# Optimization experiments

Hardware: AMD Instinct MI355X
Metric: run time of the kernel (lower is better)

## Reference

```python
import jax, jax.numpy as jnp
import numpy as np

W_IMG, H_IMG = 800.0, 600.0          # BoxList.size (w, h)
BBOX_W = (10.0, 10.0, 5.0, 5.0)      # BoxCoder weights
BBOX_CLAMP = float(np.log(1000.0 / 16.0))
SCORE_THRESH = 0.05
NMS_THRESH = 0.5
TOPN_PER_CLS = 300
DET_PER_IMG = 100


def setup_inputs() -> dict:
    key = jax.random.key(0)
    kl, kb, kp, kf = jax.random.split(key, 4)
    B, N, C, D = 2, 512, 151, 4096
    # spread logits so softmax produces scores above the 0.05 threshold
    class_logits = jax.random.normal(kl, (B, N, C), jnp.float32) * 4.0
    box_regression = jax.random.normal(kb, (B, N, C * 4), jnp.float32) * 0.2
    # valid xyxy proposal boxes inside the image
    pts = jax.random.uniform(kp, (B, N, 2, 2), jnp.float32)
    pts = pts * jnp.array([W_IMG - 1.0, H_IMG - 1.0], jnp.float32)
    lo = jnp.min(pts, axis=2)
    hi = jnp.max(pts, axis=2)
    proposal_boxes = jnp.concatenate([lo, hi], axis=-1)
    features = jax.random.normal(kf, (B, N, D), jnp.float32)
    return {"class_logits": class_logits, "box_regression": box_regression,
            "proposal_boxes": proposal_boxes, "features": features}


def decode_boxes(reg, boxes):
    wx, wy, ww, wh = BBOX_W
    widths = boxes[..., 2] - boxes[..., 0] + 1.0
    heights = boxes[..., 3] - boxes[..., 1] + 1.0
    ctr_x = boxes[..., 0] + 0.5 * widths
    ctr_y = boxes[..., 1] + 0.5 * heights
    dx = reg[..., 0] / wx
    dy = reg[..., 1] / wy
    dw = jnp.minimum(reg[..., 2] / ww, BBOX_CLAMP)
    dh = jnp.minimum(reg[..., 3] / wh, BBOX_CLAMP)
    pcx = dx * widths[..., None] + ctr_x[..., None]
    pcy = dy * heights[..., None] + ctr_y[..., None]
    pw = jnp.exp(dw) * widths[..., None]
    ph = jnp.exp(dh) * heights[..., None]
    return jnp.stack([pcx - 0.5 * pw, pcy - 0.5 * ph,
                      pcx + 0.5 * pw - 1.0, pcy + 0.5 * ph - 1.0], axis=-1)


def pairwise_iou(b):
    area = (b[:, 2] - b[:, 0] + 1.0) * (b[:, 3] - b[:, 1] + 1.0)
    xx1 = jnp.maximum(b[:, None, 0], b[None, :, 0])
    yy1 = jnp.maximum(b[:, None, 1], b[None, :, 1])
    xx2 = jnp.minimum(b[:, None, 2], b[None, :, 2])
    yy2 = jnp.minimum(b[:, None, 3], b[None, :, 3])
    inter = jnp.maximum(xx2 - xx1 + 1.0, 0.0) * jnp.maximum(yy2 - yy1 + 1.0, 0.0)
    return inter / (area[:, None] + area[None, :] - inter)


def class_nms(boxes, scores, valid):
    # Greedy NMS over one class of one image; fixed-shape, returns keep mask in
    # the ORIGINAL proposal order. `valid` = score > SCORE_THRESH prefilter.
    N = scores.shape[0]
    order = jnp.argsort(-scores)
    b = jax.lax.stop_gradient(boxes[order])
    v = valid[order]
    iou = pairwise_iou(b)
    idx = jnp.arange(N)
    def body(i, keep):
        sup = (iou[i] > NMS_THRESH) & (idx > i) & keep[i]
        return keep & ~sup
    keep = jax.lax.fori_loop(0, N, body, v)
    keep = keep & (jnp.cumsum(keep) <= TOPN_PER_CLS)  # post-NMS per-class top-n
    return jnp.zeros(N, bool).at[order].set(keep)


def reference(class_logits, box_regression, proposal_boxes, features):
    B, N, C = class_logits.shape
    prob = jax.nn.softmax(class_logits, axis=-1)                 # [B,N,C]
    reg = box_regression.reshape(B, N, C, 4)
    boxes = decode_boxes(reg, proposal_boxes)                    # [B,N,C,4]
    # clip_to_image(remove_empty=False)
    x = jnp.clip(boxes[..., 0::2], 0.0, W_IMG - 1.0)
    y = jnp.clip(boxes[..., 1::2], 0.0, H_IMG - 1.0)
    boxes = jnp.stack([x[..., 0], y[..., 0], x[..., 1], y[..., 1]], axis=-1)
    valid = prob > SCORE_THRESH                                  # [B,N,C]
    # per-(image, class) NMS, vectorized via vmap
    boxes_c = jnp.swapaxes(boxes, 1, 2)                          # [B,C,N,4]
    scores_c = jnp.swapaxes(prob, 1, 2)                          # [B,C,N]
    valid_c = jnp.swapaxes(valid, 1, 2)
    keep_c = jax.vmap(jax.vmap(class_nms))(boxes_c, scores_c, valid_c)
    keep = jnp.swapaxes(keep_c, 1, 2)                            # [B,N,C]
    keep = keep & (jnp.arange(C)[None, None, :] != 0)            # drop background
    # nms_filter_duplicates: one (score, label) per proposal
    dist_scores = prob * keep
    labels = jnp.argmax(dist_scores, axis=-1)                    # [B,N]
    scores_pre = jnp.max(dist_scores, axis=-1)                   # [B,N]
    det_valid = scores_pre > 0
    # detections_per_img cap via kth-largest threshold (only if over the cap)
    num = jnp.sum(det_valid, axis=-1)                            # [B]
    kth = jax.lax.top_k(jnp.where(det_valid, scores_pre, -1.0), DET_PER_IMG)[0][:, -1]
    thr = jnp.where(num > DET_PER_IMG, kth, -1.0)
    det_valid = det_valid & (scores_pre >= thr[:, None])
    # gather box of the winning class: boxes_per_cls[final_inds, labels_pre]
    final_boxes = jnp.take_along_axis(boxes, labels[..., None, None], axis=2)[:, :, 0, :]
    final_boxes = jnp.where(det_valid[..., None], final_boxes, 0.0)
    final_scores = jnp.where(det_valid, scores_pre, 0.0)
    final_labels = jnp.where(det_valid, labels, 0)
    nms_features = features * det_valid[..., None]               # features[orig_inds]
    return final_boxes, final_scores, final_labels, det_valid, nms_features
```

## Files before the change

kernel.cpp:

```cpp
#include <hip/hip_runtime.h>
#include <math.h>

#define Bn 2
#define Nn 512
#define Cn 151
#define Dn 4096
#define W_IMG 800.0f
#define H_IMG 600.0f
#define SCORE_T 0.05f
#define NMS_T 0.5f
#define TOPN 300
#define DETMAX 100
#define BBOX_CLAMP 4.135166556742356f

#define OFF_BOXES  ((size_t)0)
#define OFF_SCORES ((size_t)(Bn * Nn * 4))
#define OFF_LABELS (OFF_SCORES + (size_t)(Bn * Nn))
#define OFF_VALID  (OFF_LABELS + (size_t)(Bn * Nn))
#define OFF_FEATS  (OFF_VALID + (size_t)(Bn * Nn))

__device__ __forceinline__ float4 decode_clip(const float4 pr, const float4 rg) {
  const float w = pr.z - pr.x + 1.0f;
  const float h = pr.w - pr.y + 1.0f;
  const float cx = pr.x + 0.5f * w;
  const float cy = pr.y + 0.5f * h;
  const float dx = rg.x / 10.0f;
  const float dy = rg.y / 10.0f;
  const float dw = fminf(rg.z / 5.0f, BBOX_CLAMP);
  const float dh = fminf(rg.w / 5.0f, BBOX_CLAMP);
  const float pcx = dx * w + cx;
  const float pcy = dy * h + cy;
  const float pw = expf(dw) * w;
  const float ph = expf(dh) * h;
  float x1 = pcx - 0.5f * pw;
  float y1 = pcy - 0.5f * ph;
  float x2 = pcx + 0.5f * pw - 1.0f;
  float y2 = pcy + 0.5f * ph - 1.0f;
  x1 = fminf(fmaxf(x1, 0.0f), W_IMG - 1.0f);
  x2 = fminf(fmaxf(x2, 0.0f), W_IMG - 1.0f);
  y1 = fminf(fmaxf(y1, 0.0f), H_IMG - 1.0f);
  y2 = fminf(fmaxf(y2, 0.0f), H_IMG - 1.0f);
  return make_float4(x1, y1, x2, y2);
}

__global__ void kA_softmax(const float* __restrict__ logits,
                           float* __restrict__ prob_t,
                           unsigned long long* __restrict__ packed) {
  const int wave = threadIdx.x >> 6;
  const int lane = threadIdx.x & 63;
  const int bn = blockIdx.x * 4 + wave;
  const int b = bn >> 9;
  const int n = bn & (Nn - 1);

  const float* lrow = logits + (size_t)bn * Cn;
  const float l0 = lrow[lane];
  const float l1 = lrow[lane + 64];
  const float l2 = (lane + 128 < Cn) ? lrow[lane + 128] : -INFINITY;

  float mx = fmaxf(l0, fmaxf(l1, l2));
  #pragma unroll
  for (int o = 32; o > 0; o >>= 1) mx = fmaxf(mx, __shfl_xor(mx, o));

  const float e0 = expf(l0 - mx);
  const float e1 = expf(l1 - mx);
  const float e2 = (lane + 128 < Cn) ? expf(l2 - mx) : 0.0f;
  float sum = e0 + e1 + e2;
  #pragma unroll
  for (int o = 32; o > 0; o >>= 1) sum += __shfl_xor(sum, o);
  const float inv = 1.0f / sum;

  float* pt = prob_t + (size_t)b * Cn * Nn + n;
  pt[(size_t)lane * Nn] = e0 * inv;
  pt[(size_t)(lane + 64) * Nn] = e1 * inv;
  if (lane + 128 < Cn) pt[(size_t)(lane + 128) * Nn] = e2 * inv;

  if (lane == 0) packed[bn] = 0ull;
}

__global__ void kB_nms(const float* __restrict__ prob_t,
                       const float* __restrict__ reg,
                       const float* __restrict__ props,
                       unsigned long long* __restrict__ packed) {
  const int bc = blockIdx.x;
  const int b = bc / Cn;
  const int c = bc % Cn;
  const int lane = threadIdx.x;
  if (c == 0) return;

  __shared__ float ls[Nn];
  __shared__ int   ln[Nn];
  __shared__ float ss2[64];
  __shared__ int   sn2[64];
  __shared__ float fs[Nn];
  __shared__ int   fn[Nn];
  __shared__ float fb[Nn][4];
  __shared__ unsigned char kp[Nn];

  const float* col = prob_t + ((size_t)b * Cn + c) * Nn;
  int base = 0;
  #pragma unroll
  for (int j = 0; j < Nn / 64; ++j) {
    const int n = j * 64 + lane;
    const float s = col[n];
    const bool v = s > SCORE_T;
    const unsigned long long m = __ballot(v);
    if (v) {
      const int pos = base + __popcll(m & ((1ull << lane) - 1ull));
      ls[pos] = s; ln[pos] = n;
    }
    base += __popcll(m);
  }
  const int M = base;
  if (M == 0) return;
  __syncthreads();

  if (M <= 64) {
    float s = -1.0f; int n = -1;
    if (lane < M) { s = ls[lane]; n = ln[lane]; }
    int rank = 0;
    for (int j = 0; j < M; ++j) {
      const float sj = __shfl(s, j);
      const int nj = __shfl(n, j);
      if (lane < M) rank += (sj > s) || (sj == s && nj < n);
    }
    if (lane < M) { ss2[rank] = s; sn2[rank] = n; }
    __syncthreads();

    float sc = 0.0f; int sn = 0;
    float x1 = 0.0f, y1 = 0.0f, x2 = 0.0f, y2 = 0.0f;
    if (lane < M) {
      sc = ss2[lane]; sn = sn2[lane];
      const int i = b * Nn + sn;
      const float4 pr = *(const float4*)(props + (size_t)i * 4);
      const float4 rg = *(const float4*)(reg + ((size_t)i * Cn + c) * 4);
      const float4 bx = decode_clip(pr, rg);
      x1 = bx.x; y1 = bx.y; x2 = bx.z; y2 = bx.w;
    }
    const float area = (x2 - x1 + 1.0f) * (y2 - y1 + 1.0f);

    unsigned long long live = (M >= 64) ? ~0ull : ((1ull << M) - 1ull);
    int i = 0;
    while (i < 64) {
      const unsigned long long rem = live & (~0ull << i);
      if (!rem) break;
      i = __ffsll(rem) - 1;
      const float ax1 = __shfl(x1, i), ay1 = __shfl(y1, i);
      const float ax2 = __shfl(x2, i), ay2 = __shfl(y2, i);
      const float aarea = (ax2 - ax1 + 1.0f) * (ay2 - ay1 + 1.0f);
      const float xx1 = fmaxf(ax1, x1), yy1 = fmaxf(ay1, y1);
      const float xx2 = fminf(ax2, x2), yy2 = fminf(ay2, y2);
      const float inter = fmaxf(xx2 - xx1 + 1.0f, 0.0f) * fmaxf(yy2 - yy1 + 1.0f, 0.0f);
      const float iou = inter / (aarea + area - inter);
      const bool sup = (lane > i) && (lane < M) && ((live >> lane) & 1ull) && (iou > NMS_T);
      live &= ~__ballot(sup);
      ++i;
    }
    if (lane < M && ((live >> lane) & 1ull)) {
      const unsigned long long key =
          ((unsigned long long)__float_as_uint(sc) << 32) | (unsigned int)(Cn - c);
      atomicMax(&packed[(size_t)b * Nn + sn], key);
    }
  } else {
    for (int i0 = lane; i0 < M; i0 += 64) {
      const float si = ls[i0]; const int ni = ln[i0];
      int r = 0;
      for (int j = 0; j < M; ++j) {
        const float sj = ls[j]; const int nj = ln[j];
        r += (sj > si) || (sj == si && nj < ni);
      }
      fs[r] = si; fn[r] = ni;
    }
    __syncthreads();
    for (int i0 = lane; i0 < M; i0 += 64) {
      const int i = b * Nn + fn[i0];
      const float4 pr = *(const float4*)(props + (size_t)i * 4);
      const float4 rg = *(const float4*)(reg + ((size_t)i * Cn + c) * 4);
      const float4 bx = decode_clip(pr, rg);
      fb[i0][0] = bx.x; fb[i0][1] = bx.y; fb[i0][2] = bx.z; fb[i0][3] = bx.w;
      kp[i0] = 1;
    }
    __syncthreads();
    for (int i = 0; i < M; ++i) {
      if (!kp[i]) continue;
      const float ax1 = fb[i][0], ay1 = fb[i][1], ax2 = fb[i][2], ay2 = fb[i][3];
      const float aarea = (ax2 - ax1 + 1.0f) * (ay2 - ay1 + 1.0f);
      for (int t = i + 1 + lane; t < M; t += 64) {
        if (kp[t]) {
          const float bx1 = fb[t][0], by1 = fb[t][1], bx2 = fb[t][2], by2 = fb[t][3];
          const float barea = (bx2 - bx1 + 1.0f) * (by2 - by1 + 1.0f);
          const float xx1 = fmaxf(ax1, bx1), yy1 = fmaxf(ay1, by1);
          const float xx2 = fminf(ax2, bx2), yy2 = fminf(ay2, by2);
          const float inter = fmaxf(xx2 - xx1 + 1.0f, 0.0f) * fmaxf(yy2 - yy1 + 1.0f, 0.0f);
          if (inter / (aarea + barea - inter) > NMS_T) kp[t] = 0;
        }
      }
      __syncthreads();
    }
    if (lane == 0) {
      int cnt = 0;
      for (int t = 0; t < M; ++t)
        if (kp[t]) { if (++cnt > TOPN) kp[t] = 0; }
    }
    __syncthreads();
    for (int t = lane; t < M; t += 64) {
      if (kp[t]) {
        const unsigned long long key =
            ((unsigned long long)__float_as_uint(fs[t]) << 32) | (unsigned int)(Cn - c);
        atomicMax(&packed[(size_t)b * Nn + fn[t]], key);
      }
    }
  }
}

__global__ void kC_final(const unsigned long long* __restrict__ packed,
                         const float* __restrict__ reg,
                         const float* __restrict__ props,
                         float* __restrict__ out) {
  const int b = blockIdx.x;
  const int n = threadIdx.x;
  __shared__ float v[Nn];
  __shared__ int wcnt[8];
  __shared__ float sThr;

  const unsigned long long p = packed[(size_t)b * Nn + n];
  const float s = __uint_as_float((unsigned int)(p >> 32));
  const int label = (p != 0ull) ? (Cn - (int)(p & 0xFFFFFFFFull)) : 0;
  const bool pos = (s > 0.0f);
  v[n] = pos ? s : -1.0f;

  const unsigned long long bal = __ballot(pos);
  if ((n & 63) == 0) wcnt[n >> 6] = __popcll(bal);
  __syncthreads();
  int num = 0;
  #pragma unroll
  for (int i = 0; i < 8; ++i) num += wcnt[i];

  if (num > DETMAX) {
    for (int k = 2; k <= Nn; k <<= 1) {
      for (int j = k >> 1; j > 0; j >>= 1) {
        const int ixj = n ^ j;
        if (ixj > n) {
          const bool up = ((n & k) == 0);
          const float a = v[n], bb = v[ixj];
          if (up != (a > bb) && a != bb) { v[n] = bb; v[ixj] = a; }
        }
        __syncthreads();
      }
    }
    if (n == 0) sThr = v[DETMAX - 1];
  } else {
    if (n == 0) sThr = -1.0f;
  }
  __syncthreads();

  const bool valid = pos && (s >= sThr);
  const int i = b * Nn + n;
  float4 ob = make_float4(0.0f, 0.0f, 0.0f, 0.0f);
  if (valid) {
    const float4 pr = *(const float4*)(props + (size_t)i * 4);
    const float4 rg = *(const float4*)(reg + ((size_t)i * Cn + label) * 4);
    ob = decode_clip(pr, rg);
  }
  *(float4*)(out + OFF_BOXES + (size_t)i * 4) = ob;
  out[OFF_SCORES + i] = valid ? s : 0.0f;
  out[OFF_LABELS + i] = valid ? (float)label : 0.0f;
  out[OFF_VALID + i] = valid ? 1.0f : 0.0f;
}

__global__ void kD_feats(const float* __restrict__ feats,
                         const float* __restrict__ valid,
                         float* __restrict__ out) {
  const int row = blockIdx.x;
  const float m = valid[row];
  const float4* fi = (const float4*)(feats + (size_t)row * Dn);
  float4* fo = (float4*)(out + (size_t)row * Dn);
  #pragma unroll 4
  for (int t = threadIdx.x; t < Dn / 4; t += 256) {
    float4 x = fi[t];
    x.x *= m; x.y *= m; x.z *= m; x.w *= m;
    fo[t] = x;
  }
}

extern "C" void kernel_launch(void* const* d_in, const int* in_sizes, int n_in,
                              void* d_out, int out_size, void* d_ws, size_t ws_size,
                              hipStream_t stream) {
  const float* logits = (const float*)d_in[0];
  const float* reg    = (const float*)d_in[1];
  const float* props  = (const float*)d_in[2];
  const float* feats  = (const float*)d_in[3];
  float* out = (float*)d_out;

  unsigned long long* packed = (unsigned long long*)d_ws;
  float* prob_t = (float*)(packed + Bn * Nn);

  kA_softmax<<<Bn * Nn / 4, 256, 0, stream>>>(logits, prob_t, packed);
  kB_nms<<<Bn * Cn, 64, 0, stream>>>(prob_t, reg, props, packed);
  kC_final<<<Bn, Nn, 0, stream>>>(packed, reg, props, out);
  kD_feats<<<Bn * Nn, 256, 0, stream>>>(feats, out + OFF_VALID, out + OFF_FEATS);
}
```

Measured before the change: 96.98 us.

## Fuse softmax, NMS, top-k threshold and feature masking into one persistent kernel

Replaces the four separate kernel launches with a single 256-block persistent kernel. The stages are separated by a hand-written grid barrier built on atomic arrive/release flags. The per-class compaction now uses ds_permute so candidates stay in registers, and the bitonic sort that found the detection cap is replaced by a byte-wise radix select over the score bits. This is meant to remove launch gaps and the intermediate kernel boundaries. The costs are spin-wait barriers, only one block per CU, and a reliance on all 256 blocks being co-resident; the feature copy also runs at lower occupancy.

Measured after the change: 113.2 us. 1.17x slower.

```diff
diff --git a/kernel.cpp b/kernel.cpp
--- a/kernel.cpp
+++ b/kernel.cpp
@@ -12,6 +12,7 @@
 #define TOPN 300
 #define DETMAX 100
 #define BBOX_CLAMP 4.135166556742356f
+#define NBLK 256
 
 #define OFF_BOXES  ((size_t)0)
 #define OFF_SCORES ((size_t)(Bn * Nn * 4))
@@ -43,242 +44,300 @@
   return make_float4(x1, y1, x2, y2);
 }
 
-__global__ void kA_softmax(const float* __restrict__ logits,
-                           float* __restrict__ prob_t,
-                           unsigned long long* __restrict__ packed) {
-  const int wave = threadIdx.x >> 6;
-  const int lane = threadIdx.x & 63;
-  const int bn = blockIdx.x * 4 + wave;
-  const int b = bn >> 9;
-  const int n = bn & (Nn - 1);
-
-  const float* lrow = logits + (size_t)bn * Cn;
-  const float l0 = lrow[lane];
-  const float l1 = lrow[lane + 64];
-  const float l2 = (lane + 128 < Cn) ? lrow[lane + 128] : -INFINITY;
-
-  float mx = fmaxf(l0, fmaxf(l1, l2));
-  #pragma unroll
-  for (int o = 32; o > 0; o >>= 1) mx = fmaxf(mx, __shfl_xor(mx, o));
-
-  const float e0 = expf(l0 - mx);
-  const float e1 = expf(l1 - mx);
-  const float e2 = (lane + 128 < Cn) ? expf(l2 - mx) : 0.0f;
-  float sum = e0 + e1 + e2;
-  #pragma unroll
-  for (int o = 32; o > 0; o >>= 1) sum += __shfl_xor(sum, o);
-  const float inv = 1.0f / sum;
-
-  float* pt = prob_t + (size_t)b * Cn * Nn + n;
-  pt[(size_t)lane * Nn] = e0 * inv;
-  pt[(size_t)(lane + 64) * Nn] = e1 * inv;
-  if (lane + 128 < Cn) pt[(size_t)(lane + 128) * Nn] = e2 * inv;
-
-  if (lane == 0) packed[bn] = 0ull;
+__device__ __forceinline__ void grid_barrier(unsigned* arrive, unsigned* release,
+                                             unsigned phase) {
+  __syncthreads();
+  if (threadIdx.x == 0) {
+    __threadfence();
+    atomicExch(&arrive[blockIdx.x], phase);
+  }
+  if (blockIdx.x == 0) {
+    const unsigned j = threadIdx.x;
+    while (atomicAdd(&arrive[j], 0u) != phase) __builtin_amdgcn_s_sleep(1);
+    __syncthreads();
+    if (threadIdx.x == 0) atomicExch(release, phase);
+  }
+  if (threadIdx.x == 0) {
+    while (atomicAdd(release, 0u) != phase) __builtin_amdgcn_s_sleep(1);
+    __threadfence();
+  }
+  __syncthreads();
 }
 
-__global__ void kB_nms(const float* __restrict__ prob_t,
-                       const float* __restrict__ reg,
-                       const float* __restrict__ props,
-                       unsigned long long* __restrict__ packed) {
-  const int bc = blockIdx.x;
-  const int b = bc / Cn;
-  const int c = bc % Cn;
-  const int lane = threadIdx.x;
-  if (c == 0) return;
-
-  __shared__ float ls[Nn];
-  __shared__ int   ln[Nn];
-  __shared__ float ss2[64];
-  __shared__ int   sn2[64];
-  __shared__ float fs[Nn];
-  __shared__ int   fn[Nn];
-  __shared__ float fb[Nn][4];
-  __shared__ unsigned char kp[Nn];
-
-  const float* col = prob_t + ((size_t)b * Cn + c) * Nn;
-  int base = 0;
-  #pragma unroll
-  for (int j = 0; j < Nn / 64; ++j) {
-    const int n = j * 64 + lane;
-    const float s = col[n];
-    const bool v = s > SCORE_T;
-    const unsigned long long m = __ballot(v);
-    if (v) {
-      const int pos = base + __popcll(m & ((1ull << lane) - 1ull));
-      ls[pos] = s; ln[pos] = n;
-    }
-    base += __popcll(m);
-  }
-  const int M = base;
-  if (M == 0) return;
-  __syncthreads();
-
-  if (M <= 64) {
-    float s = -1.0f; int n = -1;
-    if (lane < M) { s = ls[lane]; n = ln[lane]; }
-    int rank = 0;
-    for (int j = 0; j < M; ++j) {
-      const float sj = __shfl(s, j);
-      const int nj = __shfl(n, j);
-      if (lane < M) rank += (sj > s) || (sj == s && nj < n);
-    }
-    if (lane < M) { ss2[rank] = s; sn2[rank] = n; }
+struct FallbackWS {
+  float fs[Nn];
+  int   fn[Nn];
+  float fb[Nn][4];
+  unsigned char kp[Nn];
+};
+union SharedU {
+  FallbackWS fwb[2];
+  struct { unsigned hist[256]; int red[256]; unsigned dsel[2]; } p3;
+};
+
+__global__ __launch_bounds__(256, 1) void fused_kernel(
+    const float* __restrict__ logits, const float* __restrict__ reg,
+    const float* __restrict__ props, const float* __restrict__ feats,
+    float* __restrict__ out,
+    unsigned long long* __restrict__ packed, float* __restrict__ prob_t,
+    unsigned* arrive, unsigned* release, float* __restrict__ thr) {
+  __shared__ SharedU sh;
+  const int blk = blockIdx.x;
+  const int tid = threadIdx.x;
+  const int wave = tid >> 6;
+  const int lane = tid & 63;
+
+  {
+    const int bn = wave * NBLK + blk;
+    const int b = bn >> 9;
+    const int n = bn & (Nn - 1);
+    const float* lrow = logits + (size_t)bn * Cn;
+    const float l0 = lrow[lane];
+    const float l1 = lrow[lane + 64];
+    const float l2 = (lane + 128 < Cn) ? lrow[lane + 128] : -INFINITY;
+    float mx = fmaxf(l0, fmaxf(l1, l2));
+    #pragma unroll
+    for (int o = 32; o > 0; o >>= 1) mx = fmaxf(mx, __shfl_xor(mx, o));
+    const float e0 = expf(l0 - mx);
+    const float e1 = expf(l1 - mx);
+    const float e2 = (lane + 128 < Cn) ? expf(l2 - mx) : 0.0f;
+    float sum = e0 + e1 + e2;
+    #pragma unroll
+    for (int o = 32; o > 0; o >>= 1) sum += __shfl_xor(sum, o);
+    const float inv = 1.0f / sum;
+    float* pt = prob_t + (size_t)b * Cn * Nn + n;
+    pt[(size_t)lane * Nn] = e0 * inv;
+    pt[(size_t)(lane + 64) * Nn] = e1 * inv;
+    if (lane + 128 < Cn) pt[(size_t)(lane + 128) * Nn] = e2 * inv;
+    if (lane == 0) packed[bn] = 0ull;
+  }
+  grid_barrier(arrive, release, 1u);
+
+  {
+    const int bc = wave * NBLK + blk;
+    if (bc < Bn * Cn && (bc % Cn) != 0) {
+      const int b = bc / Cn;
+      const int c = bc % Cn;
+      const float* col = prob_t + ((size_t)b * Cn + c) * Nn;
+
+      float s_acc = -1.0f; int n_acc = -1;
+      int base = 0;
+      #pragma unroll
+      for (int j = 0; j < Nn / 64; ++j) {
+        const int n = j * 64 + lane;
+        const float sv = col[n];
+        const bool v = sv > SCORE_T;
+        const unsigned long long m = __ballot(v);
+        const int cnt = __popcll(m);
+        if (cnt) {
+          const int pos = base + __popcll(m & ((1ull << lane) - 1ull));
+          const int dest = v ? (pos & 63) : 63;
+          const int rs = __builtin_amdgcn_ds_permute(dest << 2, __float_as_int(sv));
+          const int rn = __builtin_amdgcn_ds_permute(dest << 2, n);
+          if (lane >= base && lane < base + cnt) { s_acc = __int_as_float(rs); n_acc = rn; }
+          base += cnt;
+        }
+      }
+      const int M = base;
+
+      if (M > 0 && M < 64) {
+        const float s = s_acc; const int n = n_acc;
+        int rank = 0;
+        for (int j = 0; j < M; ++j) {
+          const float sj = __shfl(s, j);
+          const int nj = __shfl(n, j);
+          rank += ((sj > s) || (sj == s && nj < n)) ? 1 : 0;
+        }
+        const int rs2 = __builtin_amdgcn_ds_permute((rank & 63) << 2, __float_as_int(s));
+        const int rn2 = __builtin_amdgcn_ds_permute((rank & 63) << 2, n);
+        const float sc = __int_as_float(rs2);
+        const int sn = rn2;
+        float x1 = 0.0f, y1 = 0.0f, x2 = 0.0f, y2 = 0.0f;
+        if (lane < M) {
+          const int i = b * Nn + sn;
+          const float4 pr = ((const float4*)props)[i];
+          const float4 rg = ((const float4*)reg)[(size_t)i * Cn + c];
+          const float4 bx = decode_clip(pr, rg);
+          x1 = bx.x; y1 = bx.y; x2 = bx.z; y2 = bx.w;
+        }
+        const float area = (x2 - x1 + 1.0f) * (y2 - y1 + 1.0f);
+        unsigned long long live = (1ull << M) - 1ull;
+        int i = 0;
+        while (i < 64) {
+          const unsigned long long rem = live & (~0ull << i);
+          if (!rem) break;
+          i = __ffsll(rem) - 1;
+          const float ax1 = __shfl(x1, i), ay1 = __shfl(y1, i);
+          const float ax2 = __shfl(x2, i), ay2 = __shfl(y2, i);
+          const float aarea = (ax2 - ax1 + 1.0f) * (ay2 - ay1 + 1.0f);
+          const float xx1 = fmaxf(ax1, x1), yy1 = fmaxf(ay1, y1);
+          const float xx2 = fminf(ax2, x2), yy2 = fminf(ay2, y2);
+          const float inter = fmaxf(xx2 - xx1 + 1.0f, 0.0f) * fmaxf(yy2 - yy1 + 1.0f, 0.0f);
+          const float iou = inter / (aarea + area - inter);
+          const bool sup = (lane > i) && (lane < M) && ((live >> lane) & 1ull) && (iou > NMS_T);
+          live &= ~__ballot(sup);
+          ++i;
+        }
+        if (lane < M && ((live >> lane) & 1ull)) {
+          const unsigned long long key =
+              ((unsigned long long)__float_as_uint(sc) << 32) | (unsigned int)(Cn - c);
+          atomicMax(&packed[(size_t)b * Nn + sn], key);
+        }
+      } else if (M >= 64) {
+        FallbackWS* W = &sh.fwb[wave];
+        int b2 = 0;
+        for (int j = 0; j < Nn / 64; ++j) {
+          const int n = j * 64 + lane;
+          const float sv = col[n];
+          const bool v = sv > SCORE_T;
+          const unsigned long long m = __ballot(v);
+          if (v) {
+            const int pos = b2 + __popcll(m & ((1ull << lane) - 1ull));
+            W->fb[pos][0] = sv;
+            W->fb[pos][1] = __int_as_float(n);
+          }
+          b2 += __popcll(m);
+        }
+        __threadfence_block();
+        for (int i0 = lane; i0 < M; i0 += 64) {
+          const float si = W->fb[i0][0]; const int ni = __float_as_int(W->fb[i0][1]);
+          int r = 0;
+          for (int j = 0; j < M; ++j) {
+            const float sj = W->fb[j][0]; const int nj = __float_as_int(W->fb[j][1]);
+            r += ((sj > si) || (sj == si && nj < ni)) ? 1 : 0;
+          }
+          W->fs[r] = si; W->fn[r] = ni;
+        }
+        __threadfence_block();
+        for (int i0 = lane; i0 < M; i0 += 64) {
+          const int i = b * Nn + W->fn[i0];
+          const float4 pr = ((const float4*)props)[i];
+          const float4 rg = ((const float4*)reg)[(size_t)i * Cn + c];
+          const float4 bx = decode_clip(pr, rg);
+          W->fb[i0][0] = bx.x; W->fb[i0][1] = bx.y; W->fb[i0][2] = bx.z; W->fb[i0][3] = bx.w;
+          W->kp[i0] = 1;
+        }
+        __threadfence_block();
+        for (int i = 0; i < M; ++i) {
+          if (!W->kp[i]) continue;
+          const float ax1 = W->fb[i][0], ay1 = W->fb[i][1];
+          const float ax2 = W->fb[i][2], ay2 = W->fb[i][3];
+          const float aarea = (ax2 - ax1 + 1.0f) * (ay2 - ay1 + 1.0f);
+          for (int t = i + 1 + lane; t < M; t += 64) {
+            if (W->kp[t]) {
+              const float bx1 = W->fb[t][0], by1 = W->fb[t][1];
+              const float bx2 = W->fb[t][2], by2 = W->fb[t][3];
+              const float barea = (bx2 - bx1 + 1.0f) * (by2 - by1 + 1.0f);
+              const float xx1 = fmaxf(ax1, bx1), yy1 = fmaxf(ay1, by1);
+              const float xx2 = fminf(ax2, bx2), yy2 = fminf(ay2, by2);
+              const float inter = fmaxf(xx2 - xx1 + 1.0f, 0.0f) * fmaxf(yy2 - yy1 + 1.0f, 0.0f);
+              if (inter / (aarea + barea - inter) > NMS_T) W->kp[t] = 0;
+            }
+          }
+          __threadfence_block();
+        }
+        if (lane == 0) {
+          int cnt = 0;
+          for (int t = 0; t < M; ++t)
+            if (W->kp[t]) { if (++cnt > TOPN) W->kp[t] = 0; }
+        }
+        __threadfence_block();
+        for (int t = lane; t < M; t += 64) {
+          if (W->kp[t]) {
+            const unsigned long long key =
+                ((unsigned long long)__float_as_uint(W->fs[t]) << 32) | (unsigned int)(Cn - c);
+            atomicMax(&packed[(size_t)b * Nn + W->fn[t]], key);
+          }
+        }
+      }
+    }
+  }
+  grid_barrier(arrive, release, 2u);
+
+  if (blk < Bn) {
+    const int b = blk;
+    const unsigned long long p0 = packed[(size_t)b * Nn + tid];
+    const unsigned long long p1 = packed[(size_t)b * Nn + 256 + tid];
+    const unsigned k0 = (unsigned)(p0 >> 32);
+    const unsigned k1 = (unsigned)(p1 >> 32);
+    sh.p3.red[tid] = (k0 ? 1 : 0) + (k1 ? 1 : 0);
     __syncthreads();
-
-    float sc = 0.0f; int sn = 0;
-    float x1 = 0.0f, y1 = 0.0f, x2 = 0.0f, y2 = 0.0f;
-    if (lane < M) {
-      sc = ss2[lane]; sn = sn2[lane];
-      const int i = b * Nn + sn;
-      const float4 pr = *(const float4*)(props + (size_t)i * 4);
-      const float4 rg = *(const float4*)(reg + ((size_t)i * Cn + c) * 4);
-      const float4 bx = decode_clip(pr, rg);
-      x1 = bx.x; y1 = bx.y; x2 = bx.z; y2 = bx.w;
-    }
-    const float area = (x2 - x1 + 1.0f) * (y2 - y1 + 1.0f);
-
-    unsigned long long live = (M >= 64) ? ~0ull : ((1ull << M) - 1ull);
-    int i = 0;
-    while (i < 64) {
-      const unsigned long long rem = live & (~0ull << i);
-      if (!rem) break;
-      i = __ffsll(rem) - 1;
-      const float ax1 = __shfl(x1, i), ay1 = __shfl(y1, i);
-      const float ax2 = __shfl(x2, i), ay2 = __shfl(y2, i);
-      const float aarea = (ax2 - ax1 + 1.0f) * (ay2 - ay1 + 1.0f);
-      const float xx1 = fmaxf(ax1, x1), yy1 = fmaxf(ay1, y1);
-      const float xx2 = fminf(ax2, x2), yy2 = fminf(ay2, y2);
-      const float inter = fmaxf(xx2 - xx1 + 1.0f, 0.0f) * fmaxf(yy2 - yy1 + 1.0f, 0.0f);
-      const float iou = inter / (aarea + area - inter);
-      const bool sup = (lane > i) && (lane < M) && ((live >> lane) & 1ull) && (iou > NMS_T);
-      live &= ~__ballot(sup);
-      ++i;
-    }
-    if (lane < M && ((live >> lane) & 1ull)) {
-      const unsigned long long key =
-          ((unsigned long long)__float_as_uint(sc) << 32) | (unsigned int)(Cn - c);
-      atomicMax(&packed[(size_t)b * Nn + sn], key);
-    }
-  } else {
-    for (int i0 = lane; i0 < M; i0 += 64) {
-      const float si = ls[i0]; const int ni = ln[i0];
-      int r = 0;
-      for (int j = 0; j < M; ++j) {
-        const float sj = ls[j]; const int nj = ln[j];
-        r += (sj > si) || (sj == si && nj < ni);
-      }
-      fs[r] = si; fn[r] = ni;
-    }
-    __syncthreads();
-    for (int i0 = lane; i0 < M; i0 += 64) {
-      const int i = b * Nn + fn[i0];
-      const float4 pr = *(const float4*)(props + (size_t)i * 4);
-      const float4 rg = *(const float4*)(reg + ((size_t)i * Cn + c) * 4);
-      const float4 bx = decode_clip(pr, rg);
-      fb[i0][0] = bx.x; fb[i0][1] = bx.y; fb[i0][2] = bx.z; fb[i0][3] = bx.w;
-      kp[i0] = 1;
-    }
-    __syncthreads();
-    for (int i = 0; i < M; ++i) {
-      if (!kp[i]) continue;
-      const float ax1 = fb[i][0], ay1 = fb[i][1], ax2 = fb[i][2], ay2 = fb[i][3];
-      const float aarea = (ax2 - ax1 + 1.0f) * (ay2 - ay1 + 1.0f);
-      for (int t = i + 1 + lane; t < M; t += 64) {
-        if (kp[t]) {
-          const float bx1 = fb[t][0], by1 = fb[t][1], bx2 = fb[t][2], by2 = fb[t][3];
-          const float barea = (bx2 - bx1 + 1.0f) * (by2 - by1 + 1.0f);
-          const float xx1 = fmaxf(ax1, bx1), yy1 = fmaxf(ay1, by1);
-          const float xx2 = fminf(ax2, bx2), yy2 = fminf(ay2, by2);
-          const float inter = fmaxf(xx2 - xx1 + 1.0f, 0.0f) * fmaxf(yy2 - yy1 + 1.0f, 0.0f);
-          if (inter / (aarea + barea - inter) > NMS_T) kp[t] = 0;
-        }
-      }
+    for (int s2 = 128; s2 > 0; s2 >>= 1) {
+      if (tid < s2) sh.p3.red[tid] += sh.p3.red[tid + s2];
       __syncthreads();
     }
-    if (lane == 0) {
-      int cnt = 0;
-      for (int t = 0; t < M; ++t)
-        if (kp[t]) { if (++cnt > TOPN) kp[t] = 0; }
-    }
-    __syncthreads();
-    for (int t = lane; t < M; t += 64) {
-      if (kp[t]) {
-        const unsigned long long key =
-            ((unsigned long long)__float_as_uint(fs[t]) << 32) | (unsigned int)(Cn - c);
-        atomicMax(&packed[(size_t)b * Nn + fn[t]], key);
-      }
-    }
-  }
-}
-
-__global__ void kC_final(const unsigned long long* __restrict__ packed,
-                         const float* __restrict__ reg,
-                         const float* __restrict__ props,
-                         float* __restrict__ out) {
-  const int b = blockIdx.x;
-  const int n = threadIdx.x;
-  __shared__ float v[Nn];
-  __shared__ int wcnt[8];
-  __shared__ float sThr;
-
-  const unsigned long long p = packed[(size_t)b * Nn + n];
-  const float s = __uint_as_float((unsigned int)(p >> 32));
-  const int label = (p != 0ull) ? (Cn - (int)(p & 0xFFFFFFFFull)) : 0;
-  const bool pos = (s > 0.0f);
-  v[n] = pos ? s : -1.0f;
-
-  const unsigned long long bal = __ballot(pos);
-  if ((n & 63) == 0) wcnt[n >> 6] = __popcll(bal);
-  __syncthreads();
-  int num = 0;
-  #pragma unroll
-  for (int i = 0; i < 8; ++i) num += wcnt[i];
-
-  if (num > DETMAX) {
-    for (int k = 2; k <= Nn; k <<= 1) {
-      for (int j = k >> 1; j > 0; j >>= 1) {
-        const int ixj = n ^ j;
-        if (ixj > n) {
-          const bool up = ((n & k) == 0);
-          const float a = v[n], bb = v[ixj];
-          if (up != (a > bb) && a != bb) { v[n] = bb; v[ixj] = a; }
-        }
+    const int num = sh.p3.red[0];
+    float tv = -1.0f;
+    if (num > DETMAX) {
+      unsigned prefix = 0;
+      unsigned want = DETMAX;
+      for (int shift = 24; shift >= 0; shift -= 8) {
+        sh.p3.hist[tid] = 0;
+        __syncthreads();
+        const unsigned hm = (shift < 24) ? (0xFFFFFFFFu << (shift + 8)) : 0u;
+        if (k0 && (k0 & hm) == (prefix & hm)) atomicAdd(&sh.p3.hist[(k0 >> shift) & 0xFF], 1u);
+        if (k1 && (k1 & hm) == (prefix & hm)) atomicAdd(&sh.p3.hist[(k1 >> shift) & 0xFF], 1u);
+        __syncthreads();
+        if (tid < 64) {
+          const int l = tid;
+          const unsigned h0 = sh.p3.hist[4 * l], h1 = sh.p3.hist[4 * l + 1];
+          const unsigned h2 = sh.p3.hist[4 * l + 2], h3 = sh.p3.hist[4 * l + 3];
+          const unsigned chunk = h0 + h1 + h2 + h3;
+          unsigned suf = chunk;
+          #pragma unroll
+          for (int off = 1; off < 64; off <<= 1) {
+            const unsigned t2 = __shfl_down(suf, off);
+            if (l + off < 64) suf += t2;
+          }
+          const unsigned g3 = suf - chunk;
+          const unsigned g2 = g3 + h3;
+          const unsigned g1 = g2 + h2;
+          const unsigned g0 = g1 + h1;
+          if (g3 < want && want <= g3 + h3) { sh.p3.dsel[0] = 4 * l + 3; sh.p3.dsel[1] = want - g3; }
+          if (g2 < want && want <= g2 + h2) { sh.p3.dsel[0] = 4 * l + 2; sh.p3.dsel[1] = want - g2; }
+          if (g1 < want && want <= g1 + h1) { sh.p3.dsel[0] = 4 * l + 1; sh.p3.dsel[1] = want - g1; }
+          if (g0 < want && want <= g0 + h0) { sh.p3.dsel[0] = 4 * l + 0; sh.p3.dsel[1] = want - g0; }
+        }
+        __syncthreads();
+        prefix |= sh.p3.dsel[0] << shift;
+        want = sh.p3.dsel[1];
         __syncthreads();
       }
-    }
-    if (n == 0) sThr = v[DETMAX - 1];
-  } else {
-    if (n == 0) sThr = -1.0f;
-  }
-  __syncthreads();
-
-  const bool valid = pos && (s >= sThr);
-  const int i = b * Nn + n;
-  float4 ob = make_float4(0.0f, 0.0f, 0.0f, 0.0f);
-  if (valid) {
-    const float4 pr = *(const float4*)(props + (size_t)i * 4);
-    const float4 rg = *(const float4*)(reg + ((size_t)i * Cn + label) * 4);
-    ob = decode_clip(pr, rg);
-  }
-  *(float4*)(out + OFF_BOXES + (size_t)i * 4) = ob;
-  out[OFF_SCORES + i] = valid ? s : 0.0f;
-  out[OFF_LABELS + i] = valid ? (float)label : 0.0f;
-  out[OFF_VALID + i] = valid ? 1.0f : 0.0f;
-}
-
-__global__ void kD_feats(const float* __restrict__ feats,
-                         const float* __restrict__ valid,
-                         float* __restrict__ out) {
-  const int row = blockIdx.x;
-  const float m = valid[row];
-  const float4* fi = (const float4*)(feats + (size_t)row * Dn);
-  float4* fo = (float4*)(out + (size_t)row * Dn);
-  #pragma unroll 4
-  for (int t = threadIdx.x; t < Dn / 4; t += 256) {
-    float4 x = fi[t];
-    x.x *= m; x.y *= m; x.z *= m; x.w *= m;
-    fo[t] = x;
+      tv = __uint_as_float(prefix);
+    }
+    if (tid == 0) thr[b] = tv;
+  }
+  grid_barrier(arrive, release, 3u);
+
+  {
+    const int row = blk * 4 + wave;
+    const int b = row >> 9;
+    const unsigned long long p = packed[row];
+    const float s = __uint_as_float((unsigned)(p >> 32));
+    const int label = (p != 0ull) ? (Cn - (int)(p & 0xFFFFFFFFull)) : 0;
+    const float tb = thr[b];
+    const bool valid = (s > 0.0f) && (s >= tb);
+    if (lane == 0) {
+      float4 ob = make_float4(0.0f, 0.0f, 0.0f, 0.0f);
+      if (valid) {
+        const float4 pr = ((const float4*)props)[row];
+        const float4 rg = ((const float4*)reg)[(size_t)row * Cn + label];
+        ob = decode_clip(pr, rg);
+      }
+      ((float4*)(out + OFF_BOXES))[row] = ob;
+      out[OFF_SCORES + row] = valid ? s : 0.0f;
+      out[OFF_LABELS + row] = valid ? (float)label : 0.0f;
+      out[OFF_VALID + row] = valid ? 1.0f : 0.0f;
+    }
+    const float mval = valid ? 1.0f : 0.0f;
+    const float4* fi = (const float4*)(feats + (size_t)row * Dn);
+    float4* fo = (float4*)(out + OFF_FEATS + (size_t)row * Dn);
+    #pragma unroll
+    for (int i = 0; i < Dn / 4 / 64; ++i) {
+      float4 x = fi[i * 64 + lane];
+      x.x *= mval; x.y *= mval; x.z *= mval; x.w *= mval;
+      fo[i * 64 + lane] = x;
+    }
   }
 }
 
@@ -293,9 +352,10 @@
 
   unsigned long long* packed = (unsigned long long*)d_ws;
   float* prob_t = (float*)(packed + Bn * Nn);
-
-  kA_softmax<<<Bn * Nn / 4, 256, 0, stream>>>(logits, prob_t, packed);
-  kB_nms<<<Bn * Cn, 64, 0, stream>>>(prob_t, reg, props, packed);
-  kC_final<<<Bn, Nn, 0, stream>>>(packed, reg, props, out);
-  kD_feats<<<Bn * Nn, 256, 0, stream>>>(feats, out + OFF_VALID, out + OFF_FEATS);
+  unsigned* arrive = (unsigned*)(prob_t + (size_t)Bn * Cn * Nn);
+  unsigned* release = arrive + NBLK;
+  float* thr = (float*)(release + 1);
+
+  fused_kernel<<<NBLK, 256, 0, stream>>>(logits, reg, props, feats, out,
+                                         packed, prob_t, arrive, release, thr);
 }
```
